# Kernel optimization log

Measured on AMD Instinct MI355X. Metric: run time of the kernel, lower is better.

## Reference

```python
import jax, jax.numpy as jnp
import numpy as np

B, N, C, DK, TOPK = 4, 4096, 256, 64, 8


def setup_inputs() -> dict:
    key = jax.random.key(0)
    k1, k2, k3 = jax.random.split(key, 3)
    x = jax.random.normal(k1, (B, N, C), dtype=jnp.float32)
    # nn.Linear(channels, d_k, bias=False) weights, stored as [C, DK] for x @ W
    W_q = jax.random.normal(k2, (C, DK), dtype=jnp.float32) * (C ** -0.5)
    W_k = jax.random.normal(k3, (C, DK), dtype=jnp.float32) * (C ** -0.5)
    return {"x": x, "W_q": W_q, "W_k": W_k, "top_k": TOPK}


def reference(x, W_q, W_k, top_k):
    d_k = W_q.shape[-1]
    scale = d_k ** -0.5
    Q = x @ W_q                                   # [B, N, DK]
    K = x @ W_k                                   # [B, N, DK]
    S = jnp.einsum('bnd,bmd->bnm', Q, K) * scale  # [B, N, N]
    _, topk_idx = jax.lax.top_k(S, top_k)         # [B, N, top_k]
    n = S.shape[-1]
    # scatter True at top-k column indices per row (mirrors torch scatter_)
    row_mask = lambda idx: jnp.zeros((n,), dtype=bool).at[idx].set(True)
    mask = jax.vmap(jax.vmap(row_mask))(topk_idx)  # [B, N, N] bool
    S_masked = jnp.where(mask, S, -jnp.inf)
    A = jax.nn.softmax(S_masked, axis=-1)
    return A
```

## Files before the change

kernel.cpp:

```cpp
#include <hip/hip_runtime.h>
#include <math.h>

#define NROW 16384
#define NCOL 4096
#define CDIM 256
#define DKDIM 64
#define SCALE 0.125f

typedef float v4f __attribute__((ext_vector_type(4)));

__global__ __launch_bounds__(512, 2) void qk_proj(
    const float* __restrict__ x, const float* __restrict__ Wq,
    const float* __restrict__ Wk, float* __restrict__ Qt,
    float* __restrict__ Kt) {
  __shared__ float4 xs4[64][65];
  const int t = threadIdx.x;
  const int rb = blockIdx.x;
  {
    const float4* xg = (const float4*)(x + (size_t)rb * 64 * CDIM);
    #pragma unroll
    for (int i = 0; i < 8; ++i) {
      int idx = i * 512 + t;
      xs4[idx >> 6][idx & 63] = xg[idx];
    }
  }
  __syncthreads();

  const int lane = t & 63;
  const int wu = __builtin_amdgcn_readfirstlane(t >> 6);
  const int proj = wu >> 2;
  const int chunk = wu & 3;
  const float* __restrict__ Wp = proj ? Wk : Wq;

  float acc[16];
  #pragma unroll
  for (int j = 0; j < 16; ++j) acc[j] = 0.f;

  #pragma unroll 4
  for (int cs = 0; cs < 64; ++cs) {
    float4 xv = xs4[lane][cs];
    const float xc[4] = {xv.x, xv.y, xv.z, xv.w};
    #pragma unroll
    for (int i = 0; i < 4; ++i) {
      const float4* __restrict__ w4 =
          (const float4*)(Wp + (size_t)(cs * 4 + i) * DKDIM + chunk * 16);
      float4 wa = w4[0], wb = w4[1], wc = w4[2], wd = w4[3];
      float xi = xc[i];
      acc[0]  = fmaf(xi, wa.x, acc[0]);  acc[1]  = fmaf(xi, wa.y, acc[1]);
      acc[2]  = fmaf(xi, wa.z, acc[2]);  acc[3]  = fmaf(xi, wa.w, acc[3]);
      acc[4]  = fmaf(xi, wb.x, acc[4]);  acc[5]  = fmaf(xi, wb.y, acc[5]);
      acc[6]  = fmaf(xi, wb.z, acc[6]);  acc[7]  = fmaf(xi, wb.w, acc[7]);
      acc[8]  = fmaf(xi, wc.x, acc[8]);  acc[9]  = fmaf(xi, wc.y, acc[9]);
      acc[10] = fmaf(xi, wc.z, acc[10]); acc[11] = fmaf(xi, wc.w, acc[11]);
      acc[12] = fmaf(xi, wd.x, acc[12]); acc[13] = fmaf(xi, wd.y, acc[13]);
      acc[14] = fmaf(xi, wd.z, acc[14]); acc[15] = fmaf(xi, wd.w, acc[15]);
    }
  }

  const int gr = rb * 64 + lane;
  const int b = gr >> 12;
  const int n = gr & 4095;
  float4* __restrict__ Out4 = (float4*)(proj ? Kt : Qt);
  #pragma unroll
  for (int i = 0; i < 4; ++i) {
    int dg = chunk * 4 + i;
    float4 o = {acc[4 * i], acc[4 * i + 1], acc[4 * i + 2], acc[4 * i + 3]};
    Out4[(size_t)(b * 16 + dg) * 4096 + n] = o;
  }
}

__global__ __launch_bounds__(256, 8) void s_topk(
    const float* __restrict__ Qt, const float* __restrict__ Kt,
    float* __restrict__ out, float* __restrict__ wsv, int* __restrict__ wsi) {
  __shared__ float smem[4224];
  float4* qs = (float4*)smem;
  float (*cv)[33] = (float(*)[33])smem;
  int   (*ci)[33] = (int(*)[33])(smem + 64 * 33);

  const int t = threadIdx.x;
  const int f = blockIdx.x;
  const int xs = f & 7;
  const int i5 = f >> 3;
  const int combo = xs * 4 + (i5 >> 6);
  const int rbL = i5 & 63;
  const int b = combo >> 3;
  const int chunk = combo & 7;
  const int rb = b * 64 + rbL;
  const int lane = t & 63;
  const int wu = __builtin_amdgcn_readfirstlane(t >> 6);
  const int nb = rbL * 64;

  const float4* __restrict__ Qt4 = (const float4*)Qt;
  #pragma unroll
  for (int i = 0; i < 4; ++i) {
    int idx = i * 256 + t;
    int g = idx >> 6, row = idx & 63;
    qs[g * 64 + row] = Qt4[(size_t)(b * 16 + g) * 4096 + nb + row];
  }
  __syncthreads();

  {
    v4f z = {0.f, 0.f, 0.f, 0.f};
    v4f* o4 = (v4f*)out + (size_t)rb * 64 * 1024 + chunk * 128;
    #pragma unroll 8
    for (int i = 0; i < 32; ++i) {
      int g = i * 256 + t;
      __builtin_nontemporal_store(z, &o4[(size_t)(g >> 7) * 1024 + (g & 127)]);
    }
  }

  const float4* __restrict__ Kt4 = (const float4*)Kt;
  const int stripe = chunk * 512 + wu * 128;

  float tv[8]; int ti[8]; float tmin; int tmpos;

  auto compute8 = [&](int cb, float* acc) {
    #pragma unroll
    for (int j = 0; j < 8; ++j) acc[j] = 0.f;
    #pragma unroll 2
    for (int g = 0; g < 16; ++g) {
      float4 qf = qs[g * 64 + lane];
      const float4* __restrict__ kg =
          Kt4 + (size_t)(b * 16 + g) * 4096 + cb;
      #pragma unroll
      for (int j = 0; j < 8; ++j) {
        float4 kf = kg[j];
        acc[j] = fmaf(qf.x, kf.x, acc[j]);
        acc[j] = fmaf(qf.y, kf.y, acc[j]);
        acc[j] = fmaf(qf.z, kf.z, acc[j]);
        acc[j] = fmaf(qf.w, kf.w, acc[j]);
      }
    }
  };

  {
    float acc[8];
    compute8(stripe, acc);
    #pragma unroll
    for (int j = 0; j < 8; ++j) { tv[j] = acc[j]; ti[j] = stripe + j; }
    tmin = tv[0]; tmpos = 0;
    #pragma unroll
    for (int q2 = 1; q2 < 8; ++q2)
      if (tv[q2] < tmin) { tmin = tv[q2]; tmpos = q2; }
  }

  #pragma unroll 1
  for (int cg = 1; cg < 16; ++cg) {
    const int cb = stripe + cg * 8;
    float acc[8];
    compute8(cb, acc);

    float bv = acc[0]; int bj = 0;
    #pragma unroll
    for (int j = 1; j < 8; ++j)
      if (acc[j] > bv) { bv = acc[j]; bj = j; }

    #pragma unroll
    for (int pass = 0; pass < 2; ++pass) {
      if (__any(bv > tmin)) {
        if (bv > tmin) {
          int col = cb + bj;
          #pragma unroll
          for (int q2 = 0; q2 < 8; ++q2)
            if (q2 == tmpos) { tv[q2] = bv; ti[q2] = col; }
          tmin = tv[0]; tmpos = 0;
          #pragma unroll
          for (int q2 = 1; q2 < 8; ++q2)
            if (tv[q2] < tmin) { tmin = tv[q2]; tmpos = q2; }
          #pragma unroll
          for (int j = 0; j < 8; ++j)
            if (j == bj) acc[j] = -INFINITY;
        }
        bv = acc[0]; bj = 0;
        #pragma unroll
        for (int j = 1; j < 8; ++j)
          if (acc[j] > bv) { bv = acc[j]; bj = j; }
      }
    }
    if (__any(bv > tmin)) {
      #pragma unroll
      for (int j = 0; j < 8; ++j) {
        float v = acc[j];
        if (v > tmin) {
          int col = cb + j;
          #pragma unroll
          for (int q2 = 0; q2 < 8; ++q2)
            if (q2 == tmpos) { tv[q2] = v; ti[q2] = col; }
          tmin = tv[0]; tmpos = 0;
          #pragma unroll
          for (int q2 = 1; q2 < 8; ++q2)
            if (tv[q2] < tmin) { tmin = tv[q2]; tmpos = q2; }
        }
      }
    }
  }

  __syncthreads();
  #pragma unroll
  for (int q2 = 0; q2 < 8; ++q2) {
    cv[lane][wu * 8 + q2] = tv[q2];
    ci[lane][wu * 8 + q2] = ti[q2];
  }
  __syncthreads();
  if (t < 64) {
    float rv[8]; int rid[8];
    #pragma unroll
    for (int q2 = 0; q2 < 8; ++q2) { rv[q2] = cv[t][q2]; rid[q2] = ci[t][q2]; }
    float m = rv[0]; int mp = 0;
    #pragma unroll
    for (int q2 = 1; q2 < 8; ++q2) if (rv[q2] < m) { m = rv[q2]; mp = q2; }
    #pragma unroll
    for (int c = 8; c < 32; ++c) {
      float v = cv[t][c];
      if (v > m) {
        int col = ci[t][c];
        #pragma unroll
        for (int q2 = 0; q2 < 8; ++q2) if (q2 == mp) { rv[q2] = v; rid[q2] = col; }
        m = rv[0]; mp = 0;
        #pragma unroll
        for (int q2 = 1; q2 < 8; ++q2) if (rv[q2] < m) { m = rv[q2]; mp = q2; }
      }
    }
    size_t gr = (size_t)rb * 64 + t;
    #pragma unroll
    for (int q2 = 0; q2 < 8; ++q2) {
      wsv[gr * 64 + chunk * 8 + q2] = rv[q2];
      wsi[gr * 64 + chunk * 8 + q2] = rid[q2];
    }
  }
}

__global__ __launch_bounds__(256) void merge_scatter(
    const float* __restrict__ wsv, const int* __restrict__ wsi,
    float* __restrict__ out) {
  int row = blockIdx.x * 256 + threadIdx.x;
  const float4* v4 = (const float4*)(wsv + (size_t)row * 64);
  const int4*   i4 = (const int4*)(wsi + (size_t)row * 64);
  float rv[8]; int rid[8];
  {
    float4 a0 = v4[0], a1 = v4[1];
    int4   c0 = i4[0], c1 = i4[1];
    rv[0]=a0.x; rv[1]=a0.y; rv[2]=a0.z; rv[3]=a0.w;
    rv[4]=a1.x; rv[5]=a1.y; rv[6]=a1.z; rv[7]=a1.w;
    rid[0]=c0.x; rid[1]=c0.y; rid[2]=c0.z; rid[3]=c0.w;
    rid[4]=c1.x; rid[5]=c1.y; rid[6]=c1.z; rid[7]=c1.w;
  }
  float m = rv[0]; int mp = 0;
  #pragma unroll
  for (int q = 1; q < 8; ++q) if (rv[q] < m) { m = rv[q]; mp = q; }
  #pragma unroll 2
  for (int c4 = 2; c4 < 16; ++c4) {
    float4 a = v4[c4]; int4 ic = i4[c4];
    const float vv[4] = {a.x, a.y, a.z, a.w};
    const int   ii[4] = {ic.x, ic.y, ic.z, ic.w};
    #pragma unroll
    for (int k = 0; k < 4; ++k) {
      if (vv[k] > m) {
        #pragma unroll
        for (int q = 0; q < 8; ++q) if (q == mp) { rv[q] = vv[k]; rid[q] = ii[k]; }
        m = rv[0]; mp = 0;
        #pragma unroll
        for (int q = 1; q < 8; ++q) if (rv[q] < m) { m = rv[q]; mp = q; }
      }
    }
  }
  float vmax = rv[0];
  #pragma unroll
  for (int q = 1; q < 8; ++q) vmax = fmaxf(vmax, rv[q]);
  float e[8], s = 0.f;
  #pragma unroll
  for (int q = 0; q < 8; ++q) { e[q] = __expf((rv[q] - vmax) * SCALE); s += e[q]; }
  float inv = 1.f / s;
  float* orow = out + (size_t)row * NCOL;
  #pragma unroll
  for (int q = 0; q < 8; ++q) orow[rid[q]] = e[q] * inv;
}

extern "C" void kernel_launch(void* const* d_in, const int* in_sizes, int n_in,
                              void* d_out, int out_size, void* d_ws, size_t ws_size,
                              hipStream_t stream) {
  const float* x  = (const float*)d_in[0];
  const float* Wq = (const float*)d_in[1];
  const float* Wk = (const float*)d_in[2];
  float* out = (float*)d_out;

  char* ws = (char*)d_ws;
  float* Qt  = (float*)ws;
  float* Kt  = (float*)(ws + (size_t)NROW * DKDIM * 4);
  float* wsv = (float*)(ws + 2 * (size_t)NROW * DKDIM * 4);
  int*   wsi = (int*)  (ws + 2 * (size_t)NROW * DKDIM * 4 + (size_t)NROW * 64 * 4);

  qk_proj<<<dim3(NROW / 64), 512, 0, stream>>>(x, Wq, Wk, Qt, Kt);
  s_topk<<<2048, 256, 0, stream>>>(Qt, Kt, out, wsv, wsi);
  merge_scatter<<<NROW / 256, 256, 0, stream>>>(wsv, wsi, out);
}
```

Measured before the change: 533.4 us.

## Use bf16 MFMA for candidate scores with packed keys and fp32 rescoring

The projection now writes both row-major fp32 and bf16 copies of Q and K. The score pass uses bf16 16x16x32 MFMA instead of scalar FMAs. Each score is packed into a 32-bit key (monotone float bits in the high part, column index in the low 12 bits), and a per-thread top-8 runs over those keys in LDS to pick 64 candidates per row. A new finalize kernel recomputes the candidates exactly in fp32, takes the top 8 with wave shuffles, and scatters the softmax. The bf16 precision and key truncation can drop true top-8 entries whose scores are close to the threshold.

```diff
diff --git a/kernel.cpp b/kernel.cpp
--- a/kernel.cpp
+++ b/kernel.cpp
@@ -8,11 +8,75 @@
 #define SCALE 0.125f
 
 typedef float v4f __attribute__((ext_vector_type(4)));
+typedef __attribute__((ext_vector_type(8))) short short8v;
+typedef __attribute__((ext_vector_type(4))) float f32x4;
+
+__device__ __forceinline__ unsigned mono(float v) {
+  unsigned u = __float_as_uint(v);
+  unsigned s = (unsigned)(((int)u) >> 31);
+  return u ^ (s | 0x80000000u);
+}
+__device__ __forceinline__ float unmono(unsigned k) {
+  unsigned u = (k & 0x80000000u) ? (k ^ 0x80000000u) : ~k;
+  return __uint_as_float(u);
+}
+__device__ __forceinline__ unsigned short f2bf(float f) {
+  unsigned u = __float_as_uint(f);
+  u += 0x7FFFu + ((u >> 16) & 1u);
+  return (unsigned short)(u >> 16);
+}
+__device__ __forceinline__ unsigned umaxu(unsigned a, unsigned b) { return a > b ? a : b; }
+
+__device__ __forceinline__ void ins8(unsigned tk[8], unsigned& tmin, int& tmpos, unsigned v) {
+  #pragma unroll
+  for (int j = 0; j < 8; ++j) if (j == tmpos) tk[j] = v;
+  tmin = tk[0]; tmpos = 0;
+  #pragma unroll
+  for (int j = 1; j < 8; ++j) if (tk[j] < tmin) { tmin = tk[j]; tmpos = j; }
+}
+__device__ __forceinline__ unsigned umax8(const unsigned kv[8]) {
+  unsigned a = umaxu(umaxu(kv[0], kv[1]), umaxu(kv[2], kv[3]));
+  unsigned b = umaxu(umaxu(kv[4], kv[5]), umaxu(kv[6], kv[7]));
+  return umaxu(a, b);
+}
+__device__ __forceinline__ void seed8(const unsigned* __restrict__ sp,
+                                      unsigned tk[8], unsigned& tmin, int& tmpos) {
+  uint4 ka = *(const uint4*)(sp);
+  uint4 kb = *(const uint4*)(sp + 4);
+  tk[0] = ka.x; tk[1] = ka.y; tk[2] = ka.z; tk[3] = ka.w;
+  tk[4] = kb.x; tk[5] = kb.y; tk[6] = kb.z; tk[7] = kb.w;
+  tmin = tk[0]; tmpos = 0;
+  #pragma unroll
+  for (int j = 1; j < 8; ++j) if (tk[j] < tmin) { tmin = tk[j]; tmpos = j; }
+}
+__device__ __forceinline__ void scan8(const unsigned* __restrict__ sp,
+                                      unsigned tk[8], unsigned& tmin, int& tmpos) {
+  uint4 ka = *(const uint4*)(sp);
+  uint4 kb = *(const uint4*)(sp + 4);
+  unsigned kv[8] = {ka.x, ka.y, ka.z, ka.w, kb.x, kb.y, kb.z, kb.w};
+  unsigned gm = umax8(kv);
+  #pragma unroll
+  for (int pass = 0; pass < 2; ++pass) {
+    if (__any(gm > tmin)) {
+      if (gm > tmin) {
+        ins8(tk, tmin, tmpos, gm);
+        #pragma unroll
+        for (int j = 0; j < 8; ++j) if (kv[j] == gm) kv[j] = 0u;
+      }
+      gm = umax8(kv);
+    }
+  }
+  if (__any(gm > tmin)) {
+    #pragma unroll
+    for (int j = 0; j < 8; ++j) if (kv[j] > tmin) ins8(tk, tmin, tmpos, kv[j]);
+  }
+}
 
 __global__ __launch_bounds__(512, 2) void qk_proj(
     const float* __restrict__ x, const float* __restrict__ Wq,
     const float* __restrict__ Wk, float* __restrict__ Qt,
-    float* __restrict__ Kt) {
+    float* __restrict__ Kt, unsigned short* __restrict__ Qh,
+    unsigned short* __restrict__ Kh) {
   __shared__ float4 xs4[64][65];
   const int t = threadIdx.x;
   const int rb = blockIdx.x;
@@ -58,26 +122,30 @@
   }
 
   const int gr = rb * 64 + lane;
-  const int b = gr >> 12;
-  const int n = gr & 4095;
-  float4* __restrict__ Out4 = (float4*)(proj ? Kt : Qt);
+  float* Of = (proj ? Kt : Qt) + (size_t)gr * 64 + chunk * 16;
   #pragma unroll
   for (int i = 0; i < 4; ++i) {
-    int dg = chunk * 4 + i;
     float4 o = {acc[4 * i], acc[4 * i + 1], acc[4 * i + 2], acc[4 * i + 3]};
-    Out4[(size_t)(b * 16 + dg) * 4096 + n] = o;
-  }
-}
-
-__global__ __launch_bounds__(256, 8) void s_topk(
-    const float* __restrict__ Qt, const float* __restrict__ Kt,
-    float* __restrict__ out, float* __restrict__ wsv, int* __restrict__ wsi) {
-  __shared__ float smem[4224];
-  float4* qs = (float4*)smem;
-  float (*cv)[33] = (float(*)[33])smem;
-  int   (*ci)[33] = (int(*)[33])(smem + 64 * 33);
-
+    ((float4*)Of)[i] = o;
+  }
+  unsigned short* Oh = (proj ? Kh : Qh) + (size_t)gr * 64 + chunk * 16;
+  unsigned hp[8];
+  #pragma unroll
+  for (int i = 0; i < 8; ++i)
+    hp[i] = (unsigned)f2bf(acc[2 * i]) | ((unsigned)f2bf(acc[2 * i + 1]) << 16);
+  uint4 h0 = {hp[0], hp[1], hp[2], hp[3]};
+  uint4 h1 = {hp[4], hp[5], hp[6], hp[7]};
+  ((uint4*)Oh)[0] = h0;
+  ((uint4*)Oh)[1] = h1;
+}
+
+__global__ __launch_bounds__(256, 4) void s_cand(
+    const unsigned short* __restrict__ Qh, const unsigned short* __restrict__ Kh,
+    float* __restrict__ out, unsigned* __restrict__ wsk) {
+  __shared__ unsigned keys[4][16 * 132];
   const int t = threadIdx.x;
+  const int lane = t & 63;
+  const int w = __builtin_amdgcn_readfirstlane(t >> 6);
   const int f = blockIdx.x;
   const int xs = f & 7;
   const int i5 = f >> 3;
@@ -86,18 +154,11 @@
   const int b = combo >> 3;
   const int chunk = combo & 7;
   const int rb = b * 64 + rbL;
-  const int lane = t & 63;
-  const int wu = __builtin_amdgcn_readfirstlane(t >> 6);
-  const int nb = rbL * 64;
-
-  const float4* __restrict__ Qt4 = (const float4*)Qt;
-  #pragma unroll
-  for (int i = 0; i < 4; ++i) {
-    int idx = i * 256 + t;
-    int g = idx >> 6, row = idx & 63;
-    qs[g * 64 + row] = Qt4[(size_t)(b * 16 + g) * 4096 + nb + row];
-  }
-  __syncthreads();
+
+  const int l15 = lane & 15, lk = lane >> 4;
+  const int rowg = (b << 12) + rbL * 64 + w * 16 + l15;
+  const short8v a0 = *(const short8v*)(Qh + (size_t)rowg * 64 + lk * 8);
+  const short8v a1 = *(const short8v*)(Qh + (size_t)rowg * 64 + lk * 8 + 32);
 
   {
     v4f z = {0.f, 0.f, 0.f, 0.f};
@@ -109,171 +170,107 @@
     }
   }
 
-  const float4* __restrict__ Kt4 = (const float4*)Kt;
-  const int stripe = chunk * 512 + wu * 128;
-
-  float tv[8]; int ti[8]; float tmin; int tmpos;
-
-  auto compute8 = [&](int cb, float* acc) {
-    #pragma unroll
-    for (int j = 0; j < 8; ++j) acc[j] = 0.f;
-    #pragma unroll 2
-    for (int g = 0; g < 16; ++g) {
-      float4 qf = qs[g * 64 + lane];
-      const float4* __restrict__ kg =
-          Kt4 + (size_t)(b * 16 + g) * 4096 + cb;
+  unsigned* krow = keys[w];
+  const int myrow = lane >> 2, q = lane & 3;
+  const unsigned short* Kb = Kh + ((size_t)(b << 12)) * 64;
+
+  unsigned tk[8]; unsigned tmin; int tmpos;
+
+  #pragma unroll 1
+  for (int qt = 0; qt < 4; ++qt) {
+    const int colbase = chunk * 512 + qt * 128;
+    #pragma unroll
+    for (int ct = 0; ct < 8; ++ct) {
+      const int col = colbase + ct * 16 + l15;
+      const unsigned short* kp = Kb + (size_t)col * 64 + lk * 8;
+      const short8v b0 = *(const short8v*)(kp);
+      const short8v b1 = *(const short8v*)(kp + 32);
+      f32x4 acc = {0.f, 0.f, 0.f, 0.f};
+      acc = __builtin_amdgcn_mfma_f32_16x16x32_bf16(a0, b0, acc, 0, 0, 0);
+      acc = __builtin_amdgcn_mfma_f32_16x16x32_bf16(a1, b1, acc, 0, 0, 0);
       #pragma unroll
-      for (int j = 0; j < 8; ++j) {
-        float4 kf = kg[j];
-        acc[j] = fmaf(qf.x, kf.x, acc[j]);
-        acc[j] = fmaf(qf.y, kf.y, acc[j]);
-        acc[j] = fmaf(qf.z, kf.z, acc[j]);
-        acc[j] = fmaf(qf.w, kf.w, acc[j]);
+      for (int i = 0; i < 4; ++i) {
+        unsigned kk = (mono(acc[i]) & 0xFFFFF000u) | (unsigned)col;
+        krow[(lk * 4 + i) * 132 + ct * 16 + l15] = kk;
       }
     }
-  };
+    const unsigned* sp = krow + myrow * 132 + q * 32;
+    if (qt == 0) {
+      seed8(sp, tk, tmin, tmpos);
+      scan8(sp + 8, tk, tmin, tmpos);
+      scan8(sp + 16, tk, tmin, tmpos);
+      scan8(sp + 24, tk, tmin, tmpos);
+    } else {
+      #pragma unroll
+      for (int g = 0; g < 4; ++g) scan8(sp + 8 * g, tk, tmin, tmpos);
+    }
+  }
 
   {
-    float acc[8];
-    compute8(stripe, acc);
-    #pragma unroll
-    for (int j = 0; j < 8; ++j) { tv[j] = acc[j]; ti[j] = stripe + j; }
-    tmin = tv[0]; tmpos = 0;
-    #pragma unroll
-    for (int q2 = 1; q2 < 8; ++q2)
-      if (tv[q2] < tmin) { tmin = tv[q2]; tmpos = q2; }
-  }
-
-  #pragma unroll 1
-  for (int cg = 1; cg < 16; ++cg) {
-    const int cb = stripe + cg * 8;
-    float acc[8];
-    compute8(cb, acc);
-
-    float bv = acc[0]; int bj = 0;
-    #pragma unroll
-    for (int j = 1; j < 8; ++j)
-      if (acc[j] > bv) { bv = acc[j]; bj = j; }
-
-    #pragma unroll
-    for (int pass = 0; pass < 2; ++pass) {
-      if (__any(bv > tmin)) {
-        if (bv > tmin) {
-          int col = cb + bj;
-          #pragma unroll
-          for (int q2 = 0; q2 < 8; ++q2)
-            if (q2 == tmpos) { tv[q2] = bv; ti[q2] = col; }
-          tmin = tv[0]; tmpos = 0;
-          #pragma unroll
-          for (int q2 = 1; q2 < 8; ++q2)
-            if (tv[q2] < tmin) { tmin = tv[q2]; tmpos = q2; }
-          #pragma unroll
-          for (int j = 0; j < 8; ++j)
-            if (j == bj) acc[j] = -INFINITY;
-        }
-        bv = acc[0]; bj = 0;
-        #pragma unroll
-        for (int j = 1; j < 8; ++j)
-          if (acc[j] > bv) { bv = acc[j]; bj = j; }
-      }
-    }
-    if (__any(bv > tmin)) {
-      #pragma unroll
-      for (int j = 0; j < 8; ++j) {
-        float v = acc[j];
-        if (v > tmin) {
-          int col = cb + j;
-          #pragma unroll
-          for (int q2 = 0; q2 < 8; ++q2)
-            if (q2 == tmpos) { tv[q2] = v; ti[q2] = col; }
-          tmin = tv[0]; tmpos = 0;
-          #pragma unroll
-          for (int q2 = 1; q2 < 8; ++q2)
-            if (tv[q2] < tmin) { tmin = tv[q2]; tmpos = q2; }
-        }
-      }
-    }
-  }
-
-  __syncthreads();
-  #pragma unroll
-  for (int q2 = 0; q2 < 8; ++q2) {
-    cv[lane][wu * 8 + q2] = tv[q2];
-    ci[lane][wu * 8 + q2] = ti[q2];
-  }
-  __syncthreads();
-  if (t < 64) {
-    float rv[8]; int rid[8];
-    #pragma unroll
-    for (int q2 = 0; q2 < 8; ++q2) { rv[q2] = cv[t][q2]; rid[q2] = ci[t][q2]; }
-    float m = rv[0]; int mp = 0;
-    #pragma unroll
-    for (int q2 = 1; q2 < 8; ++q2) if (rv[q2] < m) { m = rv[q2]; mp = q2; }
-    #pragma unroll
-    for (int c = 8; c < 32; ++c) {
-      float v = cv[t][c];
-      if (v > m) {
-        int col = ci[t][c];
-        #pragma unroll
-        for (int q2 = 0; q2 < 8; ++q2) if (q2 == mp) { rv[q2] = v; rid[q2] = col; }
-        m = rv[0]; mp = 0;
-        #pragma unroll
-        for (int q2 = 1; q2 < 8; ++q2) if (rv[q2] < m) { m = rv[q2]; mp = q2; }
-      }
-    }
-    size_t gr = (size_t)rb * 64 + t;
-    #pragma unroll
-    for (int q2 = 0; q2 < 8; ++q2) {
-      wsv[gr * 64 + chunk * 8 + q2] = rv[q2];
-      wsi[gr * 64 + chunk * 8 + q2] = rid[q2];
-    }
-  }
-}
-
-__global__ __launch_bounds__(256) void merge_scatter(
-    const float* __restrict__ wsv, const int* __restrict__ wsi,
-    float* __restrict__ out) {
-  int row = blockIdx.x * 256 + threadIdx.x;
-  const float4* v4 = (const float4*)(wsv + (size_t)row * 64);
-  const int4*   i4 = (const int4*)(wsi + (size_t)row * 64);
-  float rv[8]; int rid[8];
-  {
-    float4 a0 = v4[0], a1 = v4[1];
-    int4   c0 = i4[0], c1 = i4[1];
-    rv[0]=a0.x; rv[1]=a0.y; rv[2]=a0.z; rv[3]=a0.w;
-    rv[4]=a1.x; rv[5]=a1.y; rv[6]=a1.z; rv[7]=a1.w;
-    rid[0]=c0.x; rid[1]=c0.y; rid[2]=c0.z; rid[3]=c0.w;
-    rid[4]=c1.x; rid[5]=c1.y; rid[6]=c1.z; rid[7]=c1.w;
-  }
-  float m = rv[0]; int mp = 0;
-  #pragma unroll
-  for (int q = 1; q < 8; ++q) if (rv[q] < m) { m = rv[q]; mp = q; }
-  #pragma unroll 2
-  for (int c4 = 2; c4 < 16; ++c4) {
-    float4 a = v4[c4]; int4 ic = i4[c4];
-    const float vv[4] = {a.x, a.y, a.z, a.w};
-    const int   ii[4] = {ic.x, ic.y, ic.z, ic.w};
-    #pragma unroll
-    for (int k = 0; k < 4; ++k) {
-      if (vv[k] > m) {
-        #pragma unroll
-        for (int q = 0; q < 8; ++q) if (q == mp) { rv[q] = vv[k]; rid[q] = ii[k]; }
-        m = rv[0]; mp = 0;
-        #pragma unroll
-        for (int q = 1; q < 8; ++q) if (rv[q] < m) { m = rv[q]; mp = q; }
-      }
-    }
-  }
-  float vmax = rv[0];
-  #pragma unroll
-  for (int q = 1; q < 8; ++q) vmax = fmaxf(vmax, rv[q]);
-  float e[8], s = 0.f;
-  #pragma unroll
-  for (int q = 0; q < 8; ++q) { e[q] = __expf((rv[q] - vmax) * SCALE); s += e[q]; }
-  float inv = 1.f / s;
-  float* orow = out + (size_t)row * NCOL;
-  #pragma unroll
-  for (int q = 0; q < 8; ++q) orow[rid[q]] = e[q] * inv;
+    uint4 s0 = {tk[0], tk[1], tk[2], tk[3]};
+    uint4 s1 = {tk[4], tk[5], tk[6], tk[7]};
+    uint4* mp4 = (uint4*)(krow + myrow * 36 + q * 8);
+    mp4[0] = s0; mp4[1] = s1;
+  }
+  if (lane < 16) {
+    const unsigned* mp = krow + lane * 36;
+    unsigned mt[8]; unsigned mmin; int mmpos;
+    seed8(mp, mt, mmin, mmpos);
+    scan8(mp + 8, mt, mmin, mmpos);
+    scan8(mp + 16, mt, mmin, mmpos);
+    scan8(mp + 24, mt, mmin, mmpos);
+    const int grow = (b << 12) + rbL * 64 + w * 16 + lane;
+    uint4 o0 = {mt[0], mt[1], mt[2], mt[3]};
+    uint4 o1 = {mt[4], mt[5], mt[6], mt[7]};
+    uint4* wp = (uint4*)(wsk + (size_t)grow * 64 + chunk * 8);
+    wp[0] = o0; wp[1] = o1;
+  }
+}
+
+__global__ __launch_bounds__(256) void finalize(
+    const float* __restrict__ Qt, const float* __restrict__ Kt,
+    const unsigned* __restrict__ wsk, float* __restrict__ out) {
+  const int t = threadIdx.x;
+  const int lane = t & 63;
+  const int w = t >> 6;
+  const int row = blockIdx.x * 4 + w;
+  const int b = row >> 12;
+  const unsigned key = wsk[(size_t)row * 64 + lane];
+  const int col = (int)(key & 0xFFFu);
+  const float4* Kp = (const float4*)(Kt + ((size_t)((b << 12) + col)) * 64);
+  const float4* Qp = (const float4*)(Qt + (size_t)row * 64);
+  float s = 0.f;
+  #pragma unroll
+  for (int g = 0; g < 16; ++g) {
+    float4 qf = Qp[g];
+    float4 kf = Kp[g];
+    s = fmaf(qf.x, kf.x, s);
+    s = fmaf(qf.y, kf.y, s);
+    s = fmaf(qf.z, kf.z, s);
+    s = fmaf(qf.w, kf.w, s);
+  }
+  unsigned kx = mono(s);
+  float vals[8]; int cols[8];
+  #pragma unroll
+  for (int it = 0; it < 8; ++it) {
+    unsigned m = kx;
+    #pragma unroll
+    for (int d = 1; d < 64; d <<= 1) m = umaxu(m, (unsigned)__shfl_xor((int)m, d, 64));
+    unsigned long long win = __ballot(kx == m);
+    int wl = (int)__ffsll(win) - 1;
+    cols[it] = __shfl(col, wl, 64);
+    vals[it] = unmono(m);
+    if (lane == wl) kx = 0u;
+  }
+  float e[8], sum = 0.f;
+  #pragma unroll
+  for (int it = 0; it < 8; ++it) { e[it] = __expf((vals[it] - vals[0]) * SCALE); sum += e[it]; }
+  float inv = 1.f / sum;
+  if (lane == 0) {
+    float* orow = out + ((size_t)row << 12);
+    #pragma unroll
+    for (int it = 0; it < 8; ++it) orow[cols[it]] = e[it] * inv;
+  }
 }
 
 extern "C" void kernel_launch(void* const* d_in, const int* in_sizes, int n_in,
@@ -285,12 +282,13 @@
   float* out = (float*)d_out;
 
   char* ws = (char*)d_ws;
-  float* Qt  = (float*)ws;
-  float* Kt  = (float*)(ws + (size_t)NROW * DKDIM * 4);
-  float* wsv = (float*)(ws + 2 * (size_t)NROW * DKDIM * 4);
-  int*   wsi = (int*)  (ws + 2 * (size_t)NROW * DKDIM * 4 + (size_t)NROW * 64 * 4);
-
-  qk_proj<<<dim3(NROW / 64), 512, 0, stream>>>(x, Wq, Wk, Qt, Kt);
-  s_topk<<<2048, 256, 0, stream>>>(Qt, Kt, out, wsv, wsi);
-  merge_scatter<<<NROW / 256, 256, 0, stream>>>(wsv, wsi, out);
-}
+  float* Qt = (float*)ws;
+  float* Kt = (float*)(ws + ((size_t)4 << 20));
+  unsigned short* Qh = (unsigned short*)(ws + ((size_t)8 << 20));
+  unsigned short* Kh = (unsigned short*)(ws + ((size_t)10 << 20));
+  unsigned* wsk = (unsigned*)(ws + ((size_t)12 << 20));
+
+  qk_proj<<<dim3(NROW / 64), 512, 0, stream>>>(x, Wq, Wk, Qt, Kt, Qh, Kh);
+  s_cand<<<2048, 256, 0, stream>>>(Qh, Kh, out, wsk);
+  finalize<<<NROW / 4, 256, 0, stream>>>(Qt, Kt, wsk, out);
+}
```

Measured after the change: 467.9 us. 12.3% less time.
